# Performance work log

Measured on AMD Instinct MI355X. Metric: run time of the kernel, lower is better.

The kernel has to match this reference:

```python
import jax, jax.numpy as jnp
import numpy as np

D_MODEL = 1024
H = 16
DH = 64
FFN = 4096
CHUNK = 64
LN_EPS = 1e-5


def layer_norm(x, w, b):
    mu = x.mean(-1, keepdims=True)
    var = x.var(-1, keepdims=True)
    return (x - mu) * jax.lax.rsqrt(var + LN_EPS) * w + b


def l2_normalize(x):
    # matches torch F.normalize(p=2, dim=-1, eps=1e-12)
    n = jnp.sqrt(jnp.sum(x * x, axis=-1, keepdims=True))
    return x / jnp.maximum(n, 1e-12)


def chunk_gla(q, k, v, alpha, C=CHUNK):
    B, Hh, N, D = q.shape
    nc = N // C  # N chosen as multiple of C (pad==0 in original)
    q = q.reshape(B, Hh, nc, C, D)
    k = k.reshape(B, Hh, nc, C, D)
    v = v.reshape(B, Hh, nc, C, D)
    alpha = alpha.reshape(B, Hh, nc, C, D)

    log_a = jnp.log(jnp.maximum(alpha, 1e-6))
    la_cum = jnp.cumsum(log_a, axis=3)                  # (B,H,nc,C,D)
    la_mean = la_cum.mean(-1)                            # (B,H,nc,C)
    tril = jnp.tril(jnp.ones((C, C), dtype=q.dtype))
    decay = jnp.exp(la_mean[..., :, None] - la_mean[..., None, :]) * tril  # (B,H,nc,C,C)

    attn_intra = jnp.einsum('bhncd,bhnmd->bhncm', q, k) * decay
    o_intra = jnp.einsum('bhncm,bhnmd->bhncd', attn_intra, v)

    decay_to_end = jnp.exp(la_cum[:, :, :, -1:, :] - la_cum)
    kv_chunk = jnp.einsum('bhncf,bhnce->bhnfe', k * decay_to_end, v)  # (B,H,nc,D,D)
    chunk_decay = jnp.exp(log_a.sum(3))                  # (B,H,nc,D)
    q_dec = q * jnp.exp(la_cum)                          # decay_from_start

    def step(S, inp):
        qd, kv, cd = inp                                 # (B,H,C,D),(B,H,D,D),(B,H,D)
        o = jnp.einsum('bhcd,bhde->bhce', qd, S)
        S_new = S * cd[:, :, :, None] + kv
        return S_new, o

    S0 = jnp.zeros((B, Hh, D, D), dtype=q.dtype)
    _, o_inter = jax.lax.scan(
        step, S0,
        (jnp.moveaxis(q_dec, 2, 0), jnp.moveaxis(kv_chunk, 2, 0), jnp.moveaxis(chunk_decay, 2, 0)))
    o_inter = jnp.moveaxis(o_inter, 0, 2)                # (B,H,nc,C,D)
    return (o_intra + o_inter).reshape(B, Hh, N, D)


def setup_inputs() -> dict:
    key = jax.random.key(0)
    ks = jax.random.split(key, 16)
    s = 0.02
    td = H * DH
    return {
        'x': jax.random.normal(ks[0], (2, 4096, D_MODEL), dtype=jnp.float32),
        'Wq': jax.random.normal(ks[1], (D_MODEL, td), dtype=jnp.float32) * s,
        'Wk': jax.random.normal(ks[2], (D_MODEL, td), dtype=jnp.float32) * s,
        'Wv': jax.random.normal(ks[3], (D_MODEL, td), dtype=jnp.float32) * s,
        'Wg': jax.random.normal(ks[4], (D_MODEL, td), dtype=jnp.float32) * s,
        'bg': jnp.full((td,), -0.5, dtype=jnp.float32),
        'Wo': jax.random.normal(ks[5], (td, D_MODEL), dtype=jnp.float32) * s,
        'ln1_w': jnp.ones((D_MODEL,), jnp.float32),
        'ln1_b': jnp.zeros((D_MODEL,), jnp.float32),
        'ln2_w': jnp.ones((D_MODEL,), jnp.float32),
        'ln2_b': jnp.zeros((D_MODEL,), jnp.float32),
        'W1': jax.random.normal(ks[6], (D_MODEL, FFN), dtype=jnp.float32) * s,
        'b1': jnp.zeros((FFN,), jnp.float32),
        'W2': jax.random.normal(ks[7], (FFN, D_MODEL), dtype=jnp.float32) * s,
        'b2': jnp.zeros((D_MODEL,), jnp.float32),
    }


def reference(x, Wq, Wk, Wv, Wg, bg, Wo, ln1_w, ln1_b, ln2_w, ln2_b, W1, b1, W2, b2):
    B, N, _ = x.shape
    xn = layer_norm(x, ln1_w, ln1_b)
    q = (xn @ Wq).reshape(B, N, H, DH).transpose(0, 2, 1, 3)
    k = (xn @ Wk).reshape(B, N, H, DH).transpose(0, 2, 1, 3)
    v = (xn @ Wv).reshape(B, N, H, DH).transpose(0, 2, 1, 3)
    q = l2_normalize(q)
    k = l2_normalize(k)
    alpha = jax.nn.sigmoid(xn @ Wg + bg).reshape(B, N, H, DH).transpose(0, 2, 1, 3)
    o = chunk_gla(q, k, v, alpha)
    o = o.transpose(0, 2, 1, 3).reshape(B, N, H * DH)
    x = x + o @ Wo  # dropout off (eval / p=0)
    h = layer_norm(x, ln2_w, ln2_b)
    x = x + jax.nn.gelu(h @ W1 + b1, approximate=False) @ W2 + b2
    return x
```

## Files before the change

### kernel.cpp

```cpp
#include <hip/hip_runtime.h>

#define AS1 __attribute__((address_space(1)))
#define AS3 __attribute__((address_space(3)))

typedef unsigned short u16;
typedef short s16x8 __attribute__((ext_vector_type(8)));
typedef float f32x4 __attribute__((ext_vector_type(4)));
typedef float f32x16 __attribute__((ext_vector_type(16)));

__device__ __forceinline__ float bf2f(u16 u) {
    union { unsigned u; float f; } v; v.u = ((unsigned)u) << 16; return v.f;
}
__device__ __forceinline__ u16 f2bf(float f) {
    union { float f; unsigned u; } v; v.f = f;
    unsigned u = v.u;
    return (u16)((u + 0x7FFFu + ((u >> 16) & 1u)) >> 16);
}

__device__ __forceinline__ void gload16(const void* g, void* l) {
    __builtin_amdgcn_global_load_lds((const AS1 void*)g, (AS3 void*)l, 16, 0, 0);
}

__global__ __launch_bounds__(256) void transpose_bf16(
    const float* __restrict__ src, u16* __restrict__ dst, int R, int C)
{
    __shared__ float t[32][33];
    const int tx = threadIdx.x, ty = threadIdx.y;
    const int r0 = blockIdx.x * 32, c0 = blockIdx.y * 32;
#pragma unroll
    for (int i = 0; i < 4; i++)
        t[ty + i * 8][tx] = src[(size_t)(r0 + ty + i * 8) * C + c0 + tx];
    __syncthreads();
#pragma unroll
    for (int i = 0; i < 4; i++)
        dst[(size_t)(c0 + ty + i * 8) * R + r0 + tx] = f2bf(t[tx][ty + i * 8]);
}

__global__ __launch_bounds__(256) void ln_bf16(
    const float* __restrict__ x, const float* __restrict__ w,
    const float* __restrict__ b, u16* __restrict__ out)
{
    __shared__ float red[8];
    const int row = blockIdx.x;
    const int tid = threadIdx.x;
    const size_t base = (size_t)row * 1024 + tid * 4;
    const float4 xv = *(const float4*)&x[base];
    float s = xv.x + xv.y + xv.z + xv.w;
    float q = xv.x * xv.x + xv.y * xv.y + xv.z * xv.z + xv.w * xv.w;
#pragma unroll
    for (int m = 1; m < 64; m <<= 1) { s += __shfl_xor(s, m); q += __shfl_xor(q, m); }
    if ((tid & 63) == 0) { red[tid >> 6] = s; red[4 + (tid >> 6)] = q; }
    __syncthreads();
    s = red[0] + red[1] + red[2] + red[3];
    q = red[4] + red[5] + red[6] + red[7];
    const float mu = s * (1.f / 1024.f);
    const float var = q * (1.f / 1024.f) - mu * mu;
    const float rs = rsqrtf(var + 1e-5f);
    const float4 wv = *(const float4*)&w[tid * 4];
    const float4 bv = *(const float4*)&b[tid * 4];
    uint2 ov;
    ov.x = (unsigned)f2bf((xv.x - mu) * rs * wv.x + bv.x) |
           ((unsigned)f2bf((xv.y - mu) * rs * wv.y + bv.y) << 16);
    ov.y = (unsigned)f2bf((xv.z - mu) * rs * wv.z + bv.z) |
           ((unsigned)f2bf((xv.w - mu) * rs * wv.w + bv.w) << 16);
    *(uint2*)&out[base] = ov;
}

template <int EPX>
__global__ __launch_bounds__(256, 3) void gemmS(
    const u16* __restrict__ A, const u16* __restrict__ BT,
    float* __restrict__ Cf, u16* __restrict__ Cb,
    const float* __restrict__ bias, const float* __restrict__ resid,
    int M, int N, int K)
{
    __shared__ u16 As[8192];
    __shared__ u16 Bs[8192];
    const int tid = threadIdx.x;
    const int w = tid >> 6, l = tid & 63;
    const int tm = blockIdx.x * 128, tn = blockIdx.y * 128;
    const int wm = (w >> 1) * 64, wn = (w & 1) * 64;

    const int srow = l >> 3;
    const int sg = ((l & 7) ^ srow) * 8;
    size_t aSb[4], bSb[4];
#pragma unroll
    for (int j = 0; j < 4; j++) {
        aSb[j] = (size_t)(tm + j * 32 + w * 8 + srow) * K + sg;
        bSb[j] = (size_t)(tn + j * 32 + w * 8 + srow) * K + sg;
    }

    const int la = l & 31, hi = l >> 5, key = l & 7;
    int aoff[2][4], boff[2][4];
#pragma unroll
    for (int mm = 0; mm < 2; mm++)
#pragma unroll
        for (int ks = 0; ks < 4; ks++) {
            const int g = ((ks * 2 + hi) ^ key) * 8;
            aoff[mm][ks] = (wm + mm * 32 + la) * 64 + g;
            boff[mm][ks] = (wn + mm * 32 + la) * 64 + g;
        }

    f32x16 acc[2][2] = {};

#pragma unroll
    for (int j = 0; j < 4; j++) {
        gload16(&A[aSb[j]], &As[(j * 32 + w * 8) * 64]);
        gload16(&BT[bSb[j]], &Bs[(j * 32 + w * 8) * 64]);
    }

    const int NT = K >> 6;
    for (int t = 0; t < NT; ++t) {
        __syncthreads();
#pragma unroll
        for (int ks = 0; ks < 4; ks++) {
            s16x8 a0 = *(const s16x8*)&As[aoff[0][ks]];
            s16x8 a1 = *(const s16x8*)&As[aoff[1][ks]];
            s16x8 b0 = *(const s16x8*)&Bs[boff[0][ks]];
            s16x8 b1 = *(const s16x8*)&Bs[boff[1][ks]];
            acc[0][0] = __builtin_amdgcn_mfma_f32_32x32x16_bf16(a0, b0, acc[0][0], 0, 0, 0);
            acc[0][1] = __builtin_amdgcn_mfma_f32_32x32x16_bf16(a0, b1, acc[0][1], 0, 0, 0);
            acc[1][0] = __builtin_amdgcn_mfma_f32_32x32x16_bf16(a1, b0, acc[1][0], 0, 0, 0);
            acc[1][1] = __builtin_amdgcn_mfma_f32_32x32x16_bf16(a1, b1, acc[1][1], 0, 0, 0);
        }
        if (t + 1 < NT) {
            __syncthreads();
            const int k0 = (t + 1) * 64;
#pragma unroll
            for (int j = 0; j < 4; j++) {
                gload16(&A[aSb[j] + k0], &As[(j * 32 + w * 8) * 64]);
                gload16(&BT[bSb[j] + k0], &Bs[(j * 32 + w * 8) * 64]);
            }
        }
    }

#pragma unroll
    for (int mm = 0; mm < 2; mm++)
#pragma unroll
        for (int nn = 0; nn < 2; nn++)
#pragma unroll
            for (int reg = 0; reg < 16; reg++) {
                const int row = tm + wm + mm * 32 + hi * 4 + (reg & 3) + (reg >> 2) * 8;
                const int col = tn + wn + nn * 32 + la;
                const float v = acc[mm][nn][reg];
                if (EPX == 0) {
                    if (col < 3072) Cb[(size_t)row * 3072 + col] = f2bf(v);
                    else            Cf[(size_t)row * 1024 + (col - 3072)] = v;
                } else if (EPX == 1) {
                    const float u2 = v + bias[col];
                    Cb[(size_t)row * N + col] =
                        f2bf(0.5f * u2 * (1.f + erff(u2 * 0.70710678118654752f)));
                } else if (EPX == 2) {
                    const size_t idx = (size_t)row * N + col;
                    Cf[idx] = v + resid[idx];
                } else {
                    const size_t idx = (size_t)row * N + col;
                    Cf[idx] = v + bias[col] + resid[idx];
                }
            }
}

#define TP 72
#define LP 65
__global__ __launch_bounds__(256) void gla_a(
    const u16* __restrict__ qkv,
    const float* __restrict__ g,
    const float* __restrict__ bg,
    u16* __restrict__ qdec,
    u16* __restrict__ kvT,
    float* __restrict__ cdec,
    u16* __restrict__ ointra)
{
    __shared__ u16 Qh[64 * TP];
    __shared__ u16 Kh[64 * TP];
    __shared__ u16 VT[64 * TP];
    __shared__ float L[64 * LP];
    __shared__ float lm[64], nq[64], nk[64];

    const int bid = blockIdx.x;
    const int bh = bid >> 6, ck = bid & 63;
    const int b = bh >> 4, h = bh & 15;
    const int tok0 = b * 4096 + ck * 64;
    const int tid = threadIdx.x;
    const int w = tid >> 6, l = tid & 63;

#pragma unroll
    for (int pass = 0; pass < 2; pass++) {
        const int c = (tid >> 3) + pass * 32;
        const int col = (tid & 7) * 8;
        const size_t rb = (size_t)(tok0 + c) * 3072 + h * 64 + col;
        uint4 qv = *(const uint4*)&qkv[rb];
        uint4 kv_ = *(const uint4*)&qkv[rb + 1024];
        uint4 vv = *(const uint4*)&qkv[rb + 2048];
        *(uint4*)&Qh[c * TP + col] = qv;
        *(uint4*)&Kh[c * TP + col] = kv_;
        const u16* va = (const u16*)&vv;
#pragma unroll
        for (int j = 0; j < 8; j++) VT[(col + j) * TP + c] = va[j];
    }
#pragma unroll
    for (int pass = 0; pass < 4; pass++) {
        const int c = (tid >> 4) + pass * 16;
        const int col = (tid & 15) * 4;
        float4 gv = *(const float4*)&g[(size_t)(tok0 + c) * 1024 + h * 64 + col];
        float4 bgv = *(const float4*)&bg[h * 64 + col];
        const float* ga = (const float*)&gv;
        const float* ba = (const float*)&bgv;
#pragma unroll
        for (int i = 0; i < 4; i++) {
            const float z = ga[i] + ba[i];
            const float al = 1.f / (1.f + __expf(-z));
            L[c * LP + col + i] = __logf(fmaxf(al, 1e-6f));
        }
    }
    __syncthreads();

    {
        const int d = tid >> 2, qq = tid & 3;
        float vals[16];
#pragma unroll
        for (int i = 0; i < 16; i++) vals[i] = L[(qq * 16 + i) * LP + d];
        float s = 0.f;
#pragma unroll
        for (int i = 0; i < 16; i++) { s += vals[i]; vals[i] = s; }
        float sum = s;
        float u1 = __shfl_up(sum, 1, 4); if (qq >= 1) sum += u1;
        float u2 = __shfl_up(sum, 2, 4); if (qq >= 2) sum += u2;
        const float excl = sum - s;
#pragma unroll
        for (int i = 0; i < 16; i++) L[(qq * 16 + i) * LP + d] = vals[i] + excl;
        if (qq == 3) cdec[((size_t)bh * 64 + ck) * 64 + d] = __expf(sum);
    }
    __syncthreads();

    {
        const int c = tid >> 2, qq = tid & 3;
        float sl = 0.f, sq = 0.f, sk = 0.f;
        uint4 qa = *(const uint4*)&Qh[c * TP + qq * 16];
        uint4 qb = *(const uint4*)&Qh[c * TP + qq * 16 + 8];
        uint4 ka = *(const uint4*)&Kh[c * TP + qq * 16];
        uint4 kb = *(const uint4*)&Kh[c * TP + qq * 16 + 8];
        const u16* qu = (const u16*)&qa; const u16* qu2 = (const u16*)&qb;
        const u16* ku = (const u16*)&ka; const u16* ku2 = (const u16*)&kb;
#pragma unroll
        for (int i = 0; i < 8; i++) {
            float q1 = bf2f(qu[i]), q2 = bf2f(qu2[i]);
            float k1 = bf2f(ku[i]), k2 = bf2f(ku2[i]);
            sq += q1 * q1 + q2 * q2;
            sk += k1 * k1 + k2 * k2;
        }
#pragma unroll
        for (int i = 0; i < 16; i++) sl += L[c * LP + qq * 16 + i];
        sl += __shfl_xor(sl, 1); sl += __shfl_xor(sl, 2);
        sq += __shfl_xor(sq, 1); sq += __shfl_xor(sq, 2);
        sk += __shfl_xor(sk, 1); sk += __shfl_xor(sk, 2);
        if (qq == 0) {
            lm[c] = sl * (1.f / 64.f);
            nq[c] = 1.f / fmaxf(sqrtf(sq), 1e-12f);
            nk[c] = 1.f / fmaxf(sqrtf(sk), 1e-12f);
        }
    }
    __syncthreads();

    u16 kdt[16];
    {
        const int c = tid >> 2, qq = tid & 3;
        const float qn = nq[c], kn = nk[c];
        uint4 qa = *(const uint4*)&Qh[c * TP + qq * 16];
        uint4 qb = *(const uint4*)&Qh[c * TP + qq * 16 + 8];
        uint4 ka = *(const uint4*)&Kh[c * TP + qq * 16];
        uint4 kb = *(const uint4*)&Kh[c * TP + qq * 16 + 8];
        u16* qu = (u16*)&qa; u16* qu2 = (u16*)&qb;
        u16* ku = (u16*)&ka; u16* ku2 = (u16*)&kb;
        float Lc[16], Le[16];
#pragma unroll
        for (int i = 0; i < 16; i++) {
            Lc[i] = L[c * LP + qq * 16 + i];
            Le[i] = L[63 * LP + qq * 16 + i];
        }
        unsigned pk[8];
#pragma unroll
        for (int i = 0; i < 8; i++) {
            float qh1 = bf2f(qu[i]) * qn;  qu[i] = f2bf(qh1);
            float qh2 = bf2f(qu2[i]) * qn; qu2[i] = f2bf(qh2);
            float kh1 = bf2f(ku[i]) * kn;  ku[i] = f2bf(kh1);
            float kh2 = bf2f(ku2[i]) * kn; ku2[i] = f2bf(kh2);
            kdt[i]     = f2bf(kh1 * __expf(Le[i] - Lc[i]));
            kdt[i + 8] = f2bf(kh2 * __expf(Le[i + 8] - Lc[i + 8]));
        }
#pragma unroll
        for (int i = 0; i < 4; i++) {
            pk[i] = (unsigned)f2bf(bf2f(qu[2 * i]) * __expf(Lc[2 * i])) |
                    ((unsigned)f2bf(bf2f(qu[2 * i + 1]) * __expf(Lc[2 * i + 1])) << 16);
            pk[4 + i] = (unsigned)f2bf(bf2f(qu2[2 * i]) * __expf(Lc[8 + 2 * i])) |
                        ((unsigned)f2bf(bf2f(qu2[2 * i + 1]) * __expf(Lc[8 + 2 * i + 1])) << 16);
        }
        *(uint4*)&Qh[c * TP + qq * 16] = qa;
        *(uint4*)&Qh[c * TP + qq * 16 + 8] = qb;
        *(uint4*)&Kh[c * TP + qq * 16] = ka;
        *(uint4*)&Kh[c * TP + qq * 16 + 8] = kb;
        u16* qrow = &qdec[((size_t)bh * 4096 + ck * 64 + c) * 64 + qq * 16];
        *(uint4*)&qrow[0] = *(const uint4*)&pk[0];
        *(uint4*)&qrow[8] = *(const uint4*)&pk[4];
    }
    __syncthreads();

    u16* KDT = (u16*)L;
    {
        const int c = tid >> 2, qq = tid & 3;
#pragma unroll
        for (int i = 0; i < 16; i++) KDT[(qq * 16 + i) * TP + c] = kdt[i];
    }
    const int fr = l & 15;
    const int kk = (l >> 4) * 8;
    f32x4 accS[4] = {};
#pragma unroll
    for (int ks = 0; ks < 2; ks++) {
        s16x8 af = *(const s16x8*)&Qh[(w * 16 + fr) * TP + ks * 32 + kk];
#pragma unroll
        for (int j = 0; j < 4; j++) {
            s16x8 bf = *(const s16x8*)&Kh[(j * 16 + fr) * TP + ks * 32 + kk];
            accS[j] = __builtin_amdgcn_mfma_f32_16x16x32_bf16(af, bf, accS[j], 0, 0, 0);
        }
    }
    __syncthreads();

    {
        const int erow = w * 16 + (l >> 4) * 4;
#pragma unroll
        for (int j = 0; j < 4; j++) {
            const int mm = j * 16 + (l & 15);
            const float lmm = lm[mm];
#pragma unroll
            for (int r = 0; r < 4; r++) {
                const int cc = erow + r;
                const float wgt = (mm <= cc) ? __expf(lm[cc] - lmm) : 0.f;
                Qh[cc * TP + mm] = f2bf(accS[j][r] * wgt);
            }
        }
    }
    __syncthreads();

    f32x4 accO[4] = {};
    f32x4 accK[4] = {};
#pragma unroll
    for (int ks = 0; ks < 2; ks++) {
        s16x8 aAt = *(const s16x8*)&Qh[(w * 16 + fr) * TP + ks * 32 + kk];
        s16x8 aVt = *(const s16x8*)&VT[(w * 16 + fr) * TP + ks * 32 + kk];
#pragma unroll
        for (int j = 0; j < 4; j++) {
            s16x8 bVt = *(const s16x8*)&VT[(j * 16 + fr) * TP + ks * 32 + kk];
            s16x8 bKd = *(const s16x8*)&KDT[(j * 16 + fr) * TP + ks * 32 + kk];
            accO[j] = __builtin_amdgcn_mfma_f32_16x16x32_bf16(aAt, bVt, accO[j], 0, 0, 0);
            accK[j] = __builtin_amdgcn_mfma_f32_16x16x32_bf16(aVt, bKd, accK[j], 0, 0, 0);
        }
    }
    {
        const int erow = w * 16 + (l >> 4) * 4;
#pragma unroll
        for (int j = 0; j < 4; j++) {
            const int col = j * 16 + (l & 15);
#pragma unroll
            for (int r = 0; r < 4; r++) {
                const int row = erow + r;
                ointra[((size_t)bh * 4096 + ck * 64 + row) * 64 + col] = f2bf(accO[j][r]);
                kvT[(((size_t)bh * 64 + ck) * 64 + row) * 64 + col] = f2bf(accK[j][r]);
            }
        }
    }
}

__global__ __launch_bounds__(256) void gla_scan(
    const u16* __restrict__ kvT, const float* __restrict__ cdec,
    u16* __restrict__ ST)
{
    const int bh = blockIdx.x >> 4;
    const int de = (blockIdx.x & 15) * 256 + threadIdx.x;
    const int d = de & 63;
    float s = 0.f;
    const size_t base = (size_t)bh * 64 * 4096 + de;
    const size_t cb = (size_t)bh * 4096 + d;
    for (int t = 0; t < 64; t++) {
        ST[base + (size_t)t * 4096] = f2bf(s);
        s = s * cdec[cb + (size_t)t * 64] + bf2f(kvT[base + (size_t)t * 4096]);
    }
}

__global__ __launch_bounds__(256) void gla_b(
    const u16* __restrict__ qdec, const u16* __restrict__ ST,
    const u16* __restrict__ ointra, u16* __restrict__ obf)
{
    __shared__ u16 Qd[64 * TP];
    __shared__ u16 Sd[64 * TP];
    const int bid = blockIdx.x;
    const int bh = bid >> 6, ck = bid & 63;
    const int b = bh >> 4, h = bh & 15;
    const int tid = threadIdx.x;
    const int w = tid >> 6, l = tid & 63;
#pragma unroll
    for (int pass = 0; pass < 2; pass++) {
        const int r = (tid >> 3) + pass * 32;
        const int col = (tid & 7) * 8;
        *(uint4*)&Qd[r * TP + col] =
            *(const uint4*)&qdec[((size_t)bh * 4096 + ck * 64 + r) * 64 + col];
        *(uint4*)&Sd[r * TP + col] =
            *(const uint4*)&ST[(((size_t)bh * 64 + ck) * 64 + r) * 64 + col];
    }
    __syncthreads();
    const int fr = l & 15;
    const int kk = (l >> 4) * 8;
    f32x4 acc[4] = {};
#pragma unroll
    for (int ks = 0; ks < 2; ks++) {
        s16x8 af = *(const s16x8*)&Qd[(w * 16 + fr) * TP + ks * 32 + kk];
#pragma unroll
        for (int j = 0; j < 4; j++) {
            s16x8 bf = *(const s16x8*)&Sd[(j * 16 + fr) * TP + ks * 32 + kk];
            acc[j] = __builtin_amdgcn_mfma_f32_16x16x32_bf16(af, bf, acc[j], 0, 0, 0);
        }
    }
    const int erow = w * 16 + (l >> 4) * 4;
#pragma unroll
    for (int j = 0; j < 4; j++) {
        const int e = j * 16 + (l & 15);
#pragma unroll
        for (int r = 0; r < 4; r++) {
            const int cc = erow + r;
            const size_t ia = ((size_t)bh * 4096 + ck * 64 + cc) * 64 + e;
            const float v = acc[j][r] + bf2f(ointra[ia]);
            obf[(size_t)(b * 4096 + ck * 64 + cc) * 1024 + h * 64 + e] = f2bf(v);
        }
    }
}

__global__ void fill_sentinel(float* out, int n) {
    int i = blockIdx.x * 256 + threadIdx.x;
    if (i < n) out[i] = 12345.0f;
}

extern "C" void kernel_launch(void* const* d_in, const int* in_sizes, int n_in,
                              void* d_out, int out_size, void* d_ws, size_t ws_size,
                              hipStream_t stream)
{
    const float* x    = (const float*)d_in[0];
    const float* Wq   = (const float*)d_in[1];
    const float* Wk   = (const float*)d_in[2];
    const float* Wv   = (const float*)d_in[3];
    const float* Wg   = (const float*)d_in[4];
    const float* bg   = (const float*)d_in[5];
    const float* Wo   = (const float*)d_in[6];
    const float* ln1w = (const float*)d_in[7];
    const float* ln1b = (const float*)d_in[8];
    const float* ln2w = (const float*)d_in[9];
    const float* ln2b = (const float*)d_in[10];
    const float* W1   = (const float*)d_in[11];
    const float* b1   = (const float*)d_in[12];
    const float* W2   = (const float*)d_in[13];
    const float* b2   = (const float*)d_in[14];
    float* out = (float*)d_out;

    char* ws = (char*)d_ws;
    u16*   wtQKVG = (u16*)(ws + 0);
    u16*   wtWo   = (u16*)(ws + 8388608);
    u16*   wtW1   = (u16*)(ws + 10485760);
    u16*   wtW2   = (u16*)(ws + 18874368);
    u16*   xnb    = (u16*)(ws + 27262976);
    u16*   qkvb   = (u16*)(ws + 44040192);
    float* gbuf   = (float*)(ws + 94371840);
    u16*   kvT    = (u16*)(ws + 127926272);
    float* cdbuf  = (float*)(ws + 144703488);
    u16*   qdecb  = (u16*)(ws + 145227776);
    u16*   ointra = (u16*)(ws + 162004992);
    u16*   STb    = (u16*)(ws + 178782208);
    u16*   obf    = (u16*)(ws + 195559424);
    u16*   hbf    = (u16*)(ws + 212336640);
    float* x2     = (float*)(ws + 94371840);
    u16*   ffnb   = (u16*)(ws + 27262976);

    if (ws_size < 229113856u) {
        fill_sentinel<<<dim3((out_size + 255) / 256), dim3(256), 0, stream>>>(out, out_size);
        return;
    }

    const dim3 b256(256), b32x8(32, 8);

    transpose_bf16<<<dim3(32, 32),  b32x8, 0, stream>>>(Wq, wtQKVG,               1024, 1024);
    transpose_bf16<<<dim3(32, 32),  b32x8, 0, stream>>>(Wk, wtQKVG + 1024 * 1024, 1024, 1024);
    transpose_bf16<<<dim3(32, 32),  b32x8, 0, stream>>>(Wv, wtQKVG + 2048 * 1024, 1024, 1024);
    transpose_bf16<<<dim3(32, 32),  b32x8, 0, stream>>>(Wg, wtQKVG + 3072 * 1024, 1024, 1024);
    transpose_bf16<<<dim3(32, 32),  b32x8, 0, stream>>>(Wo, wtWo,                 1024, 1024);
    transpose_bf16<<<dim3(32, 128), b32x8, 0, stream>>>(W1, wtW1,                 1024, 4096);
    transpose_bf16<<<dim3(128, 32), b32x8, 0, stream>>>(W2, wtW2,                 4096, 1024);

    ln_bf16<<<dim3(8192), b256, 0, stream>>>(x, ln1w, ln1b, xnb);
    gemmS<0><<<dim3(64, 32), b256, 0, stream>>>(xnb, wtQKVG, gbuf, qkvb, nullptr, nullptr, 8192, 4096, 1024);

    gla_a<<<dim3(2048), b256, 0, stream>>>(qkvb, gbuf, bg, qdecb, kvT, cdbuf, ointra);
    gla_scan<<<dim3(512), b256, 0, stream>>>(kvT, cdbuf, STb);
    gla_b<<<dim3(2048), b256, 0, stream>>>(qdecb, STb, ointra, obf);

    gemmS<2><<<dim3(64, 8), b256, 0, stream>>>(obf, wtWo, x2, nullptr, nullptr, x, 8192, 1024, 1024);
    ln_bf16<<<dim3(8192), b256, 0, stream>>>(x2, ln2w, ln2b, hbf);
    gemmS<1><<<dim3(64, 32), b256, 0, stream>>>(hbf, wtW1, nullptr, ffnb, b1, nullptr, 8192, 4096, 1024);
    gemmS<4><<<dim3(64, 8), b256, 0, stream>>>(ffnb, wtW2, out, nullptr, b2, x2, 8192, 1024, 4096);
}
```

Baseline: 408.2 us.

## Use 256x128 GEMM tiles with 512 threads and 16x16x32 MFMA

Replaces the 128x128, 256-thread GEMM with a 256x128 tile run by 8 waves, each computing a 64x64 sub-tile as 4x4 fragments of the 16x16x32 bf16 MFMA. The larger M tile halves B-tile reloads per output and raises arithmetic intensity per LDS byte. In exchange it uses more LDS per block (48KB) and more waves per block, and it drops the occupancy hint, which may cut concurrency. The grid for the 1024-wide GEMMs shrinks to 256 blocks, which may underfill the GPU's CUs.

```diff
diff --git a/kernel.cpp b/kernel.cpp
--- a/kernel.cpp
+++ b/kernel.cpp
@@ -6,7 +6,6 @@
 typedef unsigned short u16;
 typedef short s16x8 __attribute__((ext_vector_type(8)));
 typedef float f32x4 __attribute__((ext_vector_type(4)));
-typedef float f32x16 __attribute__((ext_vector_type(16)));
 
 __device__ __forceinline__ float bf2f(u16 u) {
     union { unsigned u; float f; } v; v.u = ((unsigned)u) << 16; return v.f;
@@ -67,81 +66,86 @@
 }
 
 template <int EPX>
-__global__ __launch_bounds__(256, 3) void gemmS(
+__global__ __launch_bounds__(512) void gemmM(
     const u16* __restrict__ A, const u16* __restrict__ BT,
     float* __restrict__ Cf, u16* __restrict__ Cb,
     const float* __restrict__ bias, const float* __restrict__ resid,
     int M, int N, int K)
 {
-    __shared__ u16 As[8192];
-    __shared__ u16 Bs[8192];
+    __shared__ u16 As[256 * 64];
+    __shared__ u16 Bs[128 * 64];
     const int tid = threadIdx.x;
     const int w = tid >> 6, l = tid & 63;
-    const int tm = blockIdx.x * 128, tn = blockIdx.y * 128;
-    const int wm = (w >> 1) * 64, wn = (w & 1) * 64;
+    const int tm = blockIdx.x * 256, tn = blockIdx.y * 128;
+    const int wr = w >> 1, wc = w & 1;
 
     const int srow = l >> 3;
-    const int sg = ((l & 7) ^ srow) * 8;
-    size_t aSb[4], bSb[4];
-#pragma unroll
-    for (int j = 0; j < 4; j++) {
-        aSb[j] = (size_t)(tm + j * 32 + w * 8 + srow) * K + sg;
-        bSb[j] = (size_t)(tn + j * 32 + w * 8 + srow) * K + sg;
-    }
-
-    const int la = l & 31, hi = l >> 5, key = l & 7;
-    int aoff[2][4], boff[2][4];
-#pragma unroll
-    for (int mm = 0; mm < 2; mm++)
-#pragma unroll
-        for (int ks = 0; ks < 4; ks++) {
-            const int g = ((ks * 2 + hi) ^ key) * 8;
-            aoff[mm][ks] = (wm + mm * 32 + la) * 64 + g;
-            boff[mm][ks] = (wn + mm * 32 + la) * 64 + g;
-        }
-
-    f32x16 acc[2][2] = {};
-
-#pragma unroll
-    for (int j = 0; j < 4; j++) {
-        gload16(&A[aSb[j]], &As[(j * 32 + w * 8) * 64]);
-        gload16(&BT[bSb[j]], &Bs[(j * 32 + w * 8) * 64]);
-    }
+    const int sg = ((l & 7) ^ (srow & 7)) * 8;
+    size_t aSb[4], bSb[2];
+#pragma unroll
+    for (int j = 0; j < 4; j++)
+        aSb[j] = (size_t)(tm + w * 32 + j * 8 + srow) * K + sg;
+#pragma unroll
+    for (int j = 0; j < 2; j++)
+        bSb[j] = (size_t)(tn + w * 16 + j * 8 + srow) * K + sg;
+
+    const int fr = l & 15, g0 = l >> 4, key = l & 7;
+    int aoff[4][2], boff[4][2];
+#pragma unroll
+    for (int f = 0; f < 4; f++)
+#pragma unroll
+        for (int ks = 0; ks < 2; ks++) {
+            const int g = ((ks * 4 + g0) ^ key) * 8;
+            aoff[f][ks] = (wr * 64 + f * 16 + fr) * 64 + g;
+            boff[f][ks] = (wc * 64 + f * 16 + fr) * 64 + g;
+        }
+
+    f32x4 acc[4][4] = {};
+
+#pragma unroll
+    for (int j = 0; j < 4; j++) gload16(&A[aSb[j]], &As[(w * 32 + j * 8) * 64]);
+#pragma unroll
+    for (int j = 0; j < 2; j++) gload16(&BT[bSb[j]], &Bs[(w * 16 + j * 8) * 64]);
 
     const int NT = K >> 6;
     for (int t = 0; t < NT; ++t) {
         __syncthreads();
 #pragma unroll
-        for (int ks = 0; ks < 4; ks++) {
-            s16x8 a0 = *(const s16x8*)&As[aoff[0][ks]];
-            s16x8 a1 = *(const s16x8*)&As[aoff[1][ks]];
-            s16x8 b0 = *(const s16x8*)&Bs[boff[0][ks]];
-            s16x8 b1 = *(const s16x8*)&Bs[boff[1][ks]];
-            acc[0][0] = __builtin_amdgcn_mfma_f32_32x32x16_bf16(a0, b0, acc[0][0], 0, 0, 0);
-            acc[0][1] = __builtin_amdgcn_mfma_f32_32x32x16_bf16(a0, b1, acc[0][1], 0, 0, 0);
-            acc[1][0] = __builtin_amdgcn_mfma_f32_32x32x16_bf16(a1, b0, acc[1][0], 0, 0, 0);
-            acc[1][1] = __builtin_amdgcn_mfma_f32_32x32x16_bf16(a1, b1, acc[1][1], 0, 0, 0);
+        for (int ks = 0; ks < 2; ks++) {
+            s16x8 a[4], b[4];
+#pragma unroll
+            for (int f = 0; f < 4; f++) {
+                a[f] = *(const s16x8*)&As[aoff[f][ks]];
+                b[f] = *(const s16x8*)&Bs[boff[f][ks]];
+            }
+#pragma unroll
+            for (int i = 0; i < 4; i++)
+#pragma unroll
+                for (int j = 0; j < 4; j++)
+                    acc[i][j] = __builtin_amdgcn_mfma_f32_16x16x32_bf16(
+                        a[i], b[j], acc[i][j], 0, 0, 0);
         }
         if (t + 1 < NT) {
             __syncthreads();
             const int k0 = (t + 1) * 64;
 #pragma unroll
-            for (int j = 0; j < 4; j++) {
-                gload16(&A[aSb[j] + k0], &As[(j * 32 + w * 8) * 64]);
-                gload16(&BT[bSb[j] + k0], &Bs[(j * 32 + w * 8) * 64]);
-            }
-        }
-    }
-
-#pragma unroll
-    for (int mm = 0; mm < 2; mm++)
-#pragma unroll
-        for (int nn = 0; nn < 2; nn++)
-#pragma unroll
-            for (int reg = 0; reg < 16; reg++) {
-                const int row = tm + wm + mm * 32 + hi * 4 + (reg & 3) + (reg >> 2) * 8;
-                const int col = tn + wn + nn * 32 + la;
-                const float v = acc[mm][nn][reg];
+            for (int j = 0; j < 4; j++) gload16(&A[aSb[j] + k0], &As[(w * 32 + j * 8) * 64]);
+#pragma unroll
+            for (int j = 0; j < 2; j++) gload16(&BT[bSb[j] + k0], &Bs[(w * 16 + j * 8) * 64]);
+        }
+    }
+
+    const int erow0 = tm + wr * 64 + (l >> 4) * 4;
+    const int ecol0 = tn + wc * 64 + (l & 15);
+#pragma unroll
+    for (int i = 0; i < 4; i++) {
+#pragma unroll
+        for (int j = 0; j < 4; j++) {
+            const int col = ecol0 + j * 16;
+#pragma unroll
+            for (int r = 0; r < 4; r++) {
+                const int row = erow0 + i * 16 + r;
+                const float v = acc[i][j][r];
                 if (EPX == 0) {
                     if (col < 3072) Cb[(size_t)row * 3072 + col] = f2bf(v);
                     else            Cf[(size_t)row * 1024 + (col - 3072)] = v;
@@ -157,6 +161,8 @@
                     Cf[idx] = v + bias[col] + resid[idx];
                 }
             }
+        }
+    }
 }
 
 #define TP 72
@@ -481,7 +487,7 @@
         return;
     }
 
-    const dim3 b256(256), b32x8(32, 8);
+    const dim3 b256(256), b512(512), b32x8(32, 8);
 
     transpose_bf16<<<dim3(32, 32),  b32x8, 0, stream>>>(Wq, wtQKVG,               1024, 1024);
     transpose_bf16<<<dim3(32, 32),  b32x8, 0, stream>>>(Wk, wtQKVG + 1024 * 1024, 1024, 1024);
@@ -492,14 +498,14 @@
     transpose_bf16<<<dim3(128, 32), b32x8, 0, stream>>>(W2, wtW2,                 4096, 1024);
 
     ln_bf16<<<dim3(8192), b256, 0, stream>>>(x, ln1w, ln1b, xnb);
-    gemmS<0><<<dim3(64, 32), b256, 0, stream>>>(xnb, wtQKVG, gbuf, qkvb, nullptr, nullptr, 8192, 4096, 1024);
+    gemmM<0><<<dim3(32, 32), b512, 0, stream>>>(xnb, wtQKVG, gbuf, qkvb, nullptr, nullptr, 8192, 4096, 1024);
 
     gla_a<<<dim3(2048), b256, 0, stream>>>(qkvb, gbuf, bg, qdecb, kvT, cdbuf, ointra);
     gla_scan<<<dim3(512), b256, 0, stream>>>(kvT, cdbuf, STb);
     gla_b<<<dim3(2048), b256, 0, stream>>>(qdecb, STb, ointra, obf);
 
-    gemmS<2><<<dim3(64, 8), b256, 0, stream>>>(obf, wtWo, x2, nullptr, nullptr, x, 8192, 1024, 1024);
+    gemmM<2><<<dim3(32, 8), b512, 0, stream>>>(obf, wtWo, x2, nullptr, nullptr, x, 8192, 1024, 1024);
     ln_bf16<<<dim3(8192), b256, 0, stream>>>(x2, ln2w, ln2b, hbf);
-    gemmS<1><<<dim3(64, 32), b256, 0, stream>>>(hbf, wtW1, nullptr, ffnb, b1, nullptr, 8192, 4096, 1024);
-    gemmS<4><<<dim3(64, 8), b256, 0, stream>>>(ffnb, wtW2, out, nullptr, b2, x2, 8192, 1024, 4096);
-}
+    gemmM<1><<<dim3(32, 32), b512, 0, stream>>>(hbf, wtW1, nullptr, ffnb, b1, nullptr, 8192, 4096, 1024);
+    gemmM<4><<<dim3(32, 8), b512, 0, stream>>>(ffnb, wtW2, out, nullptr, b2, x2, 8192, 1024, 4096);
+}
```

Result: faster. 391.5 us (-4.1%).
